# Optimization experiments

Measured on AMD Instinct MI355X. Metric: run time of the kernel, lower is better.

## Reference

```python
import jax, jax.numpy as jnp
import numpy as np

N = 100000          # nodes
E = 1600000         # edges (before self-loops)
IN = 128
H, C = 4, 32        # heads, out_channels per head
EPS = 1e-5          # BatchNorm eps
NEG_SLOPE = 0.2     # GATConv LeakyReLU slope


def setup_inputs() -> dict:
    key = jax.random.key(0)
    ks = jax.random.split(key, 8)
    return {
        "x": jax.random.normal(ks[0], (N, IN), jnp.float32),
        "edge_index": jax.random.randint(ks[1], (2, E), 0, N, dtype=jnp.int64),
        "W": jax.random.normal(ks[2], (IN, H * C), jnp.float32) * (1.0 / np.sqrt(IN)),
        "att_src": jax.random.normal(ks[3], (H, C), jnp.float32) * 0.1,
        "att_dst": jax.random.normal(ks[4], (H, C), jnp.float32) * 0.1,
        "bias": jax.random.normal(ks[5], (H * C,), jnp.float32) * 0.01,
        "gamma": jnp.ones((H * C,), jnp.float32),
        "beta": jnp.zeros((H * C,), jnp.float32),
    }


def reference(x, edge_index, W, att_src, att_dst, bias, gamma, beta):
    # --- GATConv (concat heads, add self-loops, eval-mode dropout) ---
    loop = jnp.arange(N, dtype=edge_index.dtype)
    src = jnp.concatenate([edge_index[0], loop])  # [E+N] message sources
    dst = jnp.concatenate([edge_index[1], loop])  # [E+N] message targets

    h = (x @ W).reshape(N, H, C)                       # [N,H,C]
    a_s = jnp.einsum('nhc,hc->nh', h, att_src)          # [N,H]
    a_d = jnp.einsum('nhc,hc->nh', h, att_dst)          # [N,H]

    e = a_s[src] + a_d[dst]                             # [E+N,H]
    e = jnp.where(e > 0, e, NEG_SLOPE * e)              # LeakyReLU

    # segment softmax over incoming edges of each dst node
    m = jax.ops.segment_max(e, dst, num_segments=N)     # [N,H]
    ex = jnp.exp(e - m[dst])
    den = jax.ops.segment_sum(ex, dst, num_segments=N)  # [N,H]
    alpha = ex / den[dst]                               # [E+N,H]

    out = jax.ops.segment_sum(h[src] * alpha[:, :, None], dst, num_segments=N)
    out = out.reshape(N, H * C) + bias                  # [N,128]

    # --- ELU activation ---
    out = jax.nn.elu(out)

    # --- BatchNorm1d (training-mode batch statistics, biased variance) ---
    mean = out.mean(axis=0)
    var = out.var(axis=0)
    return (out - mean) * jax.lax.rsqrt(var + EPS) * gamma + beta
```

## Files before the change

kernel.cpp:

```cpp
#include <hip/hip_runtime.h>

#define NEG 0.2f
#define MAXD 128
#define GEMM_BLOCKS 1024
#define COUNT_BLOCKS 2048

__device__ __forceinline__ float lrelu(float v) { return v > 0.f ? v : NEG * v; }

__device__ __forceinline__ unsigned f2bf(float f) {
  unsigned u = __float_as_uint(f);
  u = (u + 0x7FFFu + ((u >> 16) & 1u)) >> 16;
  return u;
}
__device__ __forceinline__ float bf_lo(unsigned u) { return __uint_as_float(u << 16); }
__device__ __forceinline__ float bf_hi(unsigned u) { return __uint_as_float(u & 0xFFFF0000u); }

typedef __attribute__((ext_vector_type(8))) short bf16x8;
typedef __attribute__((ext_vector_type(4))) float f32x4;

__global__ __launch_bounds__(256) void k_prep(const float* __restrict__ W,
                                              const float* __restrict__ att_src,
                                              const float* __restrict__ att_dst,
                                              unsigned short* __restrict__ Bext) {
  for (int id = blockIdx.x * 256 + threadIdx.x; id < 9 * 4 * 64 * 8; id += gridDim.x * 256) {
    int j = id & 7, lane = (id >> 3) & 63, kb = (id >> 9) & 3, ct = id >> 11;
    int k = kb * 32 + (lane >> 4) * 8 + j;
    int c = ct * 16 + (lane & 15);
    float v;
    if (c < 128) {
      v = W[k * 128 + c];
    } else {
      int slot = c - 128;
      int hd = slot & 3;
      const float* att = (slot < 4) ? att_src : att_dst;
      float s = 0.f;
      for (int jj = 0; jj < 32; ++jj) s = fmaf(W[k * 128 + hd * 32 + jj], att[hd * 32 + jj], s);
      v = s;
    }
    Bext[id] = (unsigned short)f2bf(v);
  }
}

__global__ __launch_bounds__(256) void k_gemm_count(
    const float* __restrict__ x, const unsigned short* __restrict__ Bext,
    unsigned* __restrict__ hb, float* __restrict__ a_s, float* __restrict__ a_d,
    int N, int ntiles,
    const int* __restrict__ ei, int* __restrict__ cnt8, int* __restrict__ rank,
    int E, int esh)
{
  const int tid = threadIdx.x;
  const int chunk = blockIdx.x >> 3;
  if (chunk % 3 == 0) {
    const int vb = (chunk / 3) * 8 + (blockIdx.x & 7);
    const bf16x8* Bfrag = reinterpret_cast<const bf16x8*>(Bext);
    const int w = tid >> 6, lane = tid & 63;
    const int r16 = lane & 15, g = lane >> 4;
    for (int tile = vb; tile < ntiles; tile += GEMM_BLOCKS) {
      int n0 = tile * 64 + w * 16;
      int rowc = min(n0 + r16, N - 1);
      const float* xp = x + (size_t)rowc * 128 + g * 8;
      bf16x8 afr[4];
#pragma unroll
      for (int kb = 0; kb < 4; ++kb) {
        float4 lo = *reinterpret_cast<const float4*>(xp + kb * 32);
        float4 hi = *reinterpret_cast<const float4*>(xp + kb * 32 + 4);
        bf16x8 t;
        t[0] = (short)f2bf(lo.x); t[1] = (short)f2bf(lo.y);
        t[2] = (short)f2bf(lo.z); t[3] = (short)f2bf(lo.w);
        t[4] = (short)f2bf(hi.x); t[5] = (short)f2bf(hi.y);
        t[6] = (short)f2bf(hi.z); t[7] = (short)f2bf(hi.w);
        afr[kb] = t;
      }
#pragma unroll
      for (int ct = 0; ct < 9; ++ct) {
        f32x4 acc = {0.f, 0.f, 0.f, 0.f};
#pragma unroll
        for (int kb = 0; kb < 4; ++kb) {
          bf16x8 bfr = Bfrag[(ct * 4 + kb) * 64 + lane];
          acc = __builtin_amdgcn_mfma_f32_16x16x32_bf16(afr[kb], bfr, acc, 0, 0, 0);
        }
        if (ct < 8) {
#pragma unroll
          for (int r = 0; r < 4; ++r) {
            int orow = n0 + g * 4 + r;
            unsigned b = f2bf(acc[r]);
            unsigned partner = __shfl_xor(b, 1);
            if (((lane & 1) == 0) && orow < N)
              hb[(size_t)orow * 64 + ct * 8 + (r16 >> 1)] = b | (partner << 16);
          }
        } else {
#pragma unroll
          for (int r = 0; r < 4; ++r) {
            int orow = n0 + g * 4 + r;
            if (r16 < 8 && orow < N) {
              if (r16 < 4) a_s[orow * 4 + r16] = acc[r];
              else         a_d[orow * 4 + (r16 - 4)] = acc[r];
            }
          }
        }
      }
    }
  } else {
    const int r = blockIdx.x & 7;
    const int cidx = chunk - 1 - (chunk / 3);
    const int qper = 1 << (esh - 2);
    const int ebase = r << esh;
    int* cpriv = cnt8 + (size_t)r * N;
    for (int ql = cidx * 256 + tid; ql < qper; ql += 256 * 256) {
      int e0 = ebase + (ql << 2);
      if (e0 >= E) break;
      if (e0 + 3 < E) {
        int4 d = *reinterpret_cast<const int4*>(ei + E + e0);
        int4 rk;
        rk.x = atomicAdd(&cpriv[d.x], 1);
        rk.y = atomicAdd(&cpriv[d.y], 1);
        rk.z = atomicAdd(&cpriv[d.z], 1);
        rk.w = atomicAdd(&cpriv[d.w], 1);
        *reinterpret_cast<int4*>(rank + e0) = rk;
      } else {
        for (int e = e0; e < E; ++e) {
          int d = ei[E + e];
          rank[e] = atomicAdd(&cpriv[d], 1);
        }
      }
    }
  }
}

__global__ __launch_bounds__(256) void k_scan1(int* __restrict__ cnt8, int* __restrict__ cnt,
                                               int* __restrict__ incl, int* __restrict__ bsum, int N) {
  __shared__ int sm[256];
  int i = blockIdx.x * 256 + threadIdx.x;
  int tot = 0;
  if (i < N) {
    int run = 0;
#pragma unroll
    for (int r = 0; r < 8; ++r) {
      int t = cnt8[(size_t)r * N + i];
      cnt8[(size_t)r * N + i] = run;
      run += t;
    }
    cnt[i] = run;
    tot = run;
  }
  sm[threadIdx.x] = tot;
  __syncthreads();
  for (int off = 1; off < 256; off <<= 1) {
    int t = (threadIdx.x >= off) ? sm[threadIdx.x - off] : 0;
    __syncthreads();
    sm[threadIdx.x] += t;
    __syncthreads();
  }
  if (i < N) incl[i] = sm[threadIdx.x];
  if (threadIdx.x == 255) bsum[blockIdx.x] = sm[255];
}

__global__ __launch_bounds__(512) void k_scan2(int* __restrict__ bsum, int nb) {
  __shared__ int sm[512];
  int v = (threadIdx.x < nb) ? bsum[threadIdx.x] : 0;
  sm[threadIdx.x] = v;
  __syncthreads();
  for (int off = 1; off < 512; off <<= 1) {
    int t = (threadIdx.x >= off) ? sm[threadIdx.x - off] : 0;
    __syncthreads();
    sm[threadIdx.x] += t;
    __syncthreads();
  }
  if (threadIdx.x < nb) bsum[threadIdx.x] = sm[threadIdx.x];
}

__global__ __launch_bounds__(256) void k_scan3(const int* __restrict__ cnt, const int* __restrict__ incl,
                                               const int* __restrict__ bsum, int* __restrict__ offs,
                                               int N, int E) {
  int i = blockIdx.x * 256 + threadIdx.x;
  if (i < N) {
    int base = (blockIdx.x > 0) ? bsum[blockIdx.x - 1] : 0;
    offs[i] = base + incl[i] - cnt[i];
  }
  if (i == 0) offs[N] = E;
}

__global__ __launch_bounds__(256) void k_scatter_rank(const int* __restrict__ ei,
                                                      const int* __restrict__ offs,
                                                      const int* __restrict__ cnt8,
                                                      const int* __restrict__ rank,
                                                      int* __restrict__ ssrc, int E, int rsize,
                                                      int esh, int N) {
  const int r = blockIdx.x & 7;
  const int lo = r * rsize, hi = lo + rsize;
  const int gtid = (blockIdx.x >> 3) * 256 + threadIdx.x;
  const int gstride = (gridDim.x >> 3) * 256;
  const int nquad = E >> 2;
  const int4* dst4 = reinterpret_cast<const int4*>(ei + E);
  for (int q = gtid; q < nquad; q += gstride) {
    int4 d = dst4[q];
    int e0 = q << 2;
    if (d.x >= lo && d.x < hi) ssrc[offs[d.x] + cnt8[(size_t)(e0 >> esh) * N + d.x] + rank[e0]]         = ei[e0];
    if (d.y >= lo && d.y < hi) ssrc[offs[d.y] + cnt8[(size_t)((e0+1) >> esh) * N + d.y] + rank[e0 + 1]] = ei[e0 + 1];
    if (d.z >= lo && d.z < hi) ssrc[offs[d.z] + cnt8[(size_t)((e0+2) >> esh) * N + d.z] + rank[e0 + 2]] = ei[e0 + 2];
    if (d.w >= lo && d.w < hi) ssrc[offs[d.w] + cnt8[(size_t)((e0+3) >> esh) * N + d.w] + rank[e0 + 3]] = ei[e0 + 3];
  }
  for (int e = (nquad << 2) + gtid; e < E; e += gstride) {
    int d = ei[E + e];
    if (d >= lo && d < hi) ssrc[offs[d] + cnt8[(size_t)(e >> esh) * N + d] + rank[e]] = ei[e];
  }
}

__global__ __launch_bounds__(256) void k_agg(
    const unsigned* __restrict__ hb, const float* __restrict__ a_s, const float* __restrict__ a_d,
    const int* __restrict__ offs, const int* __restrict__ ssrc,
    const float* __restrict__ bias, unsigned* __restrict__ preb,
    float* __restrict__ bnpart, int N)
{
  __shared__ float al[4][MAXD][4];
  __shared__ int   ls[4][MAXD];
  __shared__ float sv[4][128];
  const int wv = threadIdx.x >> 6;
  const int lane = threadIdx.x & 63;
  const int n = blockIdx.x * 4 + wv;

  if (n < N) {
    const int hsel = lane >> 4;
    const int start = offs[n], end = offs[n + 1];
    const int deg = end - start;
    const int jm = deg < MAXD ? deg : MAXD;
    float4 adv = *reinterpret_cast<const float4*>(&a_d[n * 4]);
    float4 asv = *reinterpret_cast<const float4*>(&a_s[n * 4]);
    float e0 = __expf(lrelu(asv.x + adv.x));
    float e1 = __expf(lrelu(asv.y + adv.y));
    float e2 = __expf(lrelu(asv.z + adv.z));
    float e3 = __expf(lrelu(asv.w + adv.w));
    float p0 = 0.f, p1 = 0.f, p2 = 0.f, p3 = 0.f;
    for (int j = lane; j < deg; j += 64) {
      int s = ssrc[start + j];
      float4 av = *reinterpret_cast<const float4*>(&a_s[s * 4]);
      float x0 = __expf(lrelu(av.x + adv.x));
      float x1 = __expf(lrelu(av.y + adv.y));
      float x2 = __expf(lrelu(av.z + adv.z));
      float x3 = __expf(lrelu(av.w + adv.w));
      p0 += x0; p1 += x1; p2 += x2; p3 += x3;
      if (j < MAXD) {
        float4 t = make_float4(x0, x1, x2, x3);
        *reinterpret_cast<float4*>(&al[wv][j][0]) = t;
        ls[wv][j] = s;
      }
    }
#pragma unroll
    for (int off = 32; off >= 1; off >>= 1) {
      p0 += __shfl_xor(p0, off);
      p1 += __shfl_xor(p1, off);
      p2 += __shfl_xor(p2, off);
      p3 += __shfl_xor(p3, off);
    }
    float rden0 = 1.f / (p0 + e0), rden1 = 1.f / (p1 + e1);
    float rden2 = 1.f / (p2 + e2), rden3 = 1.f / (p3 + e3);
    for (int j = lane; j < jm; j += 64) {
      float4 t = *reinterpret_cast<float4*>(&al[wv][j][0]);
      t.x *= rden0; t.y *= rden1; t.z *= rden2; t.w *= rden3;
      *reinterpret_cast<float4*>(&al[wv][j][0]) = t;
    }
    float ad_c = (hsel < 2) ? (hsel == 0 ? adv.x : adv.y) : (hsel == 2 ? adv.z : adv.w);
    float rden = (hsel < 2) ? (hsel == 0 ? rden0 : rden1) : (hsel == 2 ? rden2 : rden3);
    float esf = (hsel < 2) ? (hsel == 0 ? e0 : e1) : (hsel == 2 ? e2 : e3);
    unsigned us = hb[(size_t)n * 64 + lane];
    float wself = esf * rden;
    float acc0 = wself * bf_lo(us);
    float acc1 = wself * bf_hi(us);
    int j = 0;
    for (; j + 8 <= jm; j += 8) {
      int4 sA = *reinterpret_cast<int4*>(&ls[wv][j]);
      int4 sB = *reinterpret_cast<int4*>(&ls[wv][j + 4]);
      unsigned u0 = hb[(size_t)sA.x * 64 + lane];
      unsigned u1 = hb[(size_t)sA.y * 64 + lane];
      unsigned u2 = hb[(size_t)sA.z * 64 + lane];
      unsigned u3 = hb[(size_t)sA.w * 64 + lane];
      unsigned u4 = hb[(size_t)sB.x * 64 + lane];
      unsigned u5 = hb[(size_t)sB.y * 64 + lane];
      unsigned u6 = hb[(size_t)sB.z * 64 + lane];
      unsigned u7 = hb[(size_t)sB.w * 64 + lane];
      float w0 = al[wv][j][hsel];
      float w1 = al[wv][j + 1][hsel];
      float w2 = al[wv][j + 2][hsel];
      float w3 = al[wv][j + 3][hsel];
      float w4 = al[wv][j + 4][hsel];
      float w5 = al[wv][j + 5][hsel];
      float w6 = al[wv][j + 6][hsel];
      float w7 = al[wv][j + 7][hsel];
      acc0 = fmaf(w0, bf_lo(u0), acc0);
      acc1 = fmaf(w0, bf_hi(u0), acc1);
      acc0 = fmaf(w1, bf_lo(u1), acc0);
      acc1 = fmaf(w1, bf_hi(u1), acc1);
      acc0 = fmaf(w2, bf_lo(u2), acc0);
      acc1 = fmaf(w2, bf_hi(u2), acc1);
      acc0 = fmaf(w3, bf_lo(u3), acc0);
      acc1 = fmaf(w3, bf_hi(u3), acc1);
      acc0 = fmaf(w4, bf_lo(u4), acc0);
      acc1 = fmaf(w4, bf_hi(u4), acc1);
      acc0 = fmaf(w5, bf_lo(u5), acc0);
      acc1 = fmaf(w5, bf_hi(u5), acc1);
      acc0 = fmaf(w6, bf_lo(u6), acc0);
      acc1 = fmaf(w6, bf_hi(u6), acc1);
      acc0 = fmaf(w7, bf_lo(u7), acc0);
      acc1 = fmaf(w7, bf_hi(u7), acc1);
    }
    for (; j + 4 <= jm; j += 4) {
      int4 s4 = *reinterpret_cast<int4*>(&ls[wv][j]);
      unsigned u0 = hb[(size_t)s4.x * 64 + lane];
      unsigned u1 = hb[(size_t)s4.y * 64 + lane];
      unsigned u2 = hb[(size_t)s4.z * 64 + lane];
      unsigned u3 = hb[(size_t)s4.w * 64 + lane];
      float w0 = al[wv][j][hsel];
      float w1 = al[wv][j + 1][hsel];
      float w2 = al[wv][j + 2][hsel];
      float w3 = al[wv][j + 3][hsel];
      acc0 = fmaf(w0, bf_lo(u0), acc0);
      acc1 = fmaf(w0, bf_hi(u0), acc1);
      acc0 = fmaf(w1, bf_lo(u1), acc0);
      acc1 = fmaf(w1, bf_hi(u1), acc1);
      acc0 = fmaf(w2, bf_lo(u2), acc0);
      acc1 = fmaf(w2, bf_hi(u2), acc1);
      acc0 = fmaf(w3, bf_lo(u3), acc0);
      acc1 = fmaf(w3, bf_hi(u3), acc1);
    }
    for (; j < jm; ++j) {
      int s = ls[wv][j];
      float w = al[wv][j][hsel];
      unsigned u = hb[(size_t)s * 64 + lane];
      acc0 = fmaf(w, bf_lo(u), acc0);
      acc1 = fmaf(w, bf_hi(u), acc1);
    }
    for (int jj = MAXD; jj < deg; ++jj) {
      int s = ssrc[start + jj];
      float q = a_s[s * 4 + hsel];
      unsigned u = hb[(size_t)s * 64 + lane];
      float w = __expf(lrelu(q + ad_c)) * rden;
      acc0 = fmaf(w, bf_lo(u), acc0);
      acc1 = fmaf(w, bf_hi(u), acc1);
    }
    float2 bv = *reinterpret_cast<const float2*>(&bias[2 * lane]);
    float o0 = acc0 + bv.x;
    float o1 = acc1 + bv.y;
    o0 = o0 > 0.f ? o0 : expm1f(o0);
    o1 = o1 > 0.f ? o1 : expm1f(o1);
    preb[(size_t)n * 64 + lane] = f2bf(o0) | (f2bf(o1) << 16);
    sv[wv][2 * lane] = o0;
    sv[wv][2 * lane + 1] = o1;
  } else {
    sv[wv][2 * lane] = 0.f;
    sv[wv][2 * lane + 1] = 0.f;
  }
  __syncthreads();
  int t = threadIdx.x;
  if (t < 128) {
    float s = 0.f, q = 0.f;
#pragma unroll
    for (int w2 = 0; w2 < 4; ++w2) {
      float v = sv[w2][t];
      s += v;
      q = fmaf(v, v, q);
    }
    float* slot = bnpart + (size_t)(blockIdx.x & 63) * 256;
    atomicAdd(&slot[t], s);
    atomicAdd(&slot[128 + t], q);
  }
}

__global__ void k_bnfinal(const float* __restrict__ bnpart,
                          const float* __restrict__ gamma, const float* __restrict__ beta,
                          float* __restrict__ sc, float* __restrict__ sh, int N) {
  int c = threadIdx.x;
  float s = 0.f, q = 0.f;
  for (int p = 0; p < 64; ++p) {
    s += bnpart[p * 256 + c];
    q += bnpart[p * 256 + 128 + c];
  }
  float invn = 1.f / (float)N;
  float mean = s * invn;
  float var = q * invn - mean * mean;
  float scl = gamma[c] * rsqrtf(var + 1e-5f);
  sc[c] = scl;
  sh[c] = beta[c] - mean * scl;
}

__global__ __launch_bounds__(256) void k_bnapply(const unsigned* __restrict__ preb,
                                                 float* __restrict__ out,
                                                 const float* __restrict__ sc,
                                                 const float* __restrict__ sh, int npair2) {
  int i = blockIdx.x * blockDim.x + threadIdx.x;
  if (i >= npair2) return;
  uint2 u = reinterpret_cast<const uint2*>(preb)[i];
  int p0 = i * 2;
  int c0 = (p0 & 63) * 2;
  float4 scv = *reinterpret_cast<const float4*>(&sc[c0]);
  float4 shv = *reinterpret_cast<const float4*>(&sh[c0]);
  float4 v;
  v.x = fmaf(bf_lo(u.x), scv.x, shv.x);
  v.y = fmaf(bf_hi(u.x), scv.y, shv.y);
  v.z = fmaf(bf_lo(u.y), scv.z, shv.z);
  v.w = fmaf(bf_hi(u.y), scv.w, shv.w);
  reinterpret_cast<float4*>(out)[i] = v;
}

extern "C" void kernel_launch(void* const* d_in, const int* in_sizes, int n_in,
                              void* d_out, int out_size, void* d_ws, size_t ws_size,
                              hipStream_t stream) {
  const float* x = (const float*)d_in[0];
  const int* ei = (const int*)d_in[1];
  const float* W = (const float*)d_in[2];
  const float* att_src = (const float*)d_in[3];
  const float* att_dst = (const float*)d_in[4];
  const float* bias = (const float*)d_in[5];
  const float* gamma = (const float*)d_in[6];
  const float* beta = (const float*)d_in[7];
  float* out = (float*)d_out;

  const int N = in_sizes[0] / 128;
  const int E = in_sizes[1] / 2;

  char* ws = (char*)d_ws;
  size_t off = 0;
  auto alloc = [&](size_t bytes) {
    void* p = ws + off;
    off = (off + bytes + 255) & ~(size_t)255;
    return p;
  };
  unsigned* hb = (unsigned*)alloc((size_t)N * 64 * 4);
  float* a_s = (float*)alloc((size_t)N * 4 * 4);
  float* a_d = (float*)alloc((size_t)N * 4 * 4);
  int* cnt = (int*)alloc((size_t)N * 4);
  int* incl = (int*)alloc((size_t)N * 4);
  int* offs = (int*)alloc((size_t)(N + 1) * 4);
  int* bsum = (int*)alloc(512 * 4);
  int* rank = (int*)alloc((size_t)E * 4);
  int* ssrc = (int*)alloc((size_t)E * 4);
  unsigned* preb = (unsigned*)alloc((size_t)N * 64 * 4);
  float* bnpart = (float*)alloc(64 * 256 * 4);
  float* sc = (float*)alloc(128 * 4);
  float* sh = (float*)alloc(128 * 4);
  unsigned short* Bext = (unsigned short*)alloc(9 * 4 * 64 * 8 * 2);
  (void)n_in; (void)out_size; (void)ws_size;

  int* cnt8 = (int*)preb;

  int esh = 10;
  while (((E + (1 << esh) - 1) >> esh) > 8) ++esh;

  hipMemsetAsync(cnt8, 0, (size_t)N * 8 * 4, stream);
  hipMemsetAsync(bnpart, 0, 64 * 256 * 4, stream);

  k_prep<<<9, 256, 0, stream>>>(W, att_src, att_dst, Bext);

  int ntiles = (N + 63) / 64;
  k_gemm_count<<<GEMM_BLOCKS + COUNT_BLOCKS, 256, 0, stream>>>(
      x, Bext, hb, a_s, a_d, N, ntiles, ei, cnt8, rank, E, esh);

  int nb = (N + 255) / 256;
  k_scan1<<<nb, 256, 0, stream>>>(cnt8, cnt, incl, bsum, N);
  k_scan2<<<1, 512, 0, stream>>>(bsum, nb);
  k_scan3<<<nb, 256, 0, stream>>>(cnt, incl, bsum, offs, N, E);

  int rsize = (N + 7) / 8;
  k_scatter_rank<<<2048, 256, 0, stream>>>(ei, offs, cnt8, rank, ssrc, E, rsize, esh, N);

  k_agg<<<(N + 3) / 4, 256, 0, stream>>>(hb, a_s, a_d, offs, ssrc, bias, preb, bnpart, N);

  k_bnfinal<<<1, 128, 0, stream>>>(bnpart, gamma, beta, sc, sh, N);

  int npair2 = N * 32;
  k_bnapply<<<(npair2 + 255) / 256, 256, 0, stream>>>(preb, out, sc, sh, npair2);
}
```

Baseline: 234.0 us.

## Fuse memsets into prep, merge scan passes, fold offsets into per-slice counts

Replaces the two memset calls with zeroing loops inside the prep kernel, which now runs on 64 blocks. The second and third scan passes are merged into one kernel, where each block reduces the preceding block sums itself. That kernel also adds the node offset into each of the eight per-slice count arrays, so the scatter reads one index instead of two and loads ranks as int4. Together these cut launch count and global traffic in the CSR build, at the cost of each scan block doing a redundant reduction over up to about 390 block sums. The aggregation kernel also switches to 32-bit shift indexing for its gathers.

```diff
diff --git a/kernel.cpp b/kernel.cpp
--- a/kernel.cpp
+++ b/kernel.cpp
@@ -21,8 +21,12 @@
 __global__ __launch_bounds__(256) void k_prep(const float* __restrict__ W,
                                               const float* __restrict__ att_src,
                                               const float* __restrict__ att_dst,
-                                              unsigned short* __restrict__ Bext) {
-  for (int id = blockIdx.x * 256 + threadIdx.x; id < 9 * 4 * 64 * 8; id += gridDim.x * 256) {
+                                              unsigned short* __restrict__ Bext,
+                                              int* __restrict__ cnt8, float* __restrict__ bnpart,
+                                              int N) {
+  const int gtid = blockIdx.x * 256 + threadIdx.x;
+  const int gstride = gridDim.x * 256;
+  for (int id = gtid; id < 9 * 4 * 64 * 8; id += gstride) {
     int j = id & 7, lane = (id >> 3) & 63, kb = (id >> 9) & 3, ct = id >> 11;
     int k = kb * 32 + (lane >> 4) * 8 + j;
     int c = ct * 16 + (lane & 15);
@@ -39,6 +43,8 @@
     }
     Bext[id] = (unsigned short)f2bf(v);
   }
+  for (int i = gtid; i < N * 8; i += gstride) cnt8[i] = 0;
+  for (int i = gtid; i < 64 * 256; i += gstride) bnpart[i] = 0.f;
 }
 
 __global__ __launch_bounds__(256) void k_gemm_count(
@@ -86,7 +92,7 @@
             unsigned b = f2bf(acc[r]);
             unsigned partner = __shfl_xor(b, 1);
             if (((lane & 1) == 0) && orow < N)
-              hb[(size_t)orow * 64 + ct * 8 + (r16 >> 1)] = b | (partner << 16);
+              hb[((size_t)orow << 6) + ct * 8 + (r16 >> 1)] = b | (partner << 16);
           }
         } else {
 #pragma unroll
@@ -127,8 +133,8 @@
   }
 }
 
-__global__ __launch_bounds__(256) void k_scan1(int* __restrict__ cnt8, int* __restrict__ cnt,
-                                               int* __restrict__ incl, int* __restrict__ bsum, int N) {
+__global__ __launch_bounds__(256) void k_scan1(int* __restrict__ cnt8, int* __restrict__ excl,
+                                               int* __restrict__ bsum, int N) {
   __shared__ int sm[256];
   int i = blockIdx.x * 256 + threadIdx.x;
   int tot = 0;
@@ -140,7 +146,6 @@
       cnt8[(size_t)r * N + i] = run;
       run += t;
     }
-    cnt[i] = run;
     tot = run;
   }
   sm[threadIdx.x] = tot;
@@ -151,37 +156,36 @@
     sm[threadIdx.x] += t;
     __syncthreads();
   }
-  if (i < N) incl[i] = sm[threadIdx.x];
+  if (i < N) excl[i] = sm[threadIdx.x] - tot;
   if (threadIdx.x == 255) bsum[blockIdx.x] = sm[255];
 }
 
-__global__ __launch_bounds__(512) void k_scan2(int* __restrict__ bsum, int nb) {
-  __shared__ int sm[512];
-  int v = (threadIdx.x < nb) ? bsum[threadIdx.x] : 0;
-  sm[threadIdx.x] = v;
+__global__ __launch_bounds__(256) void k_scan23(const int* __restrict__ excl,
+                                                const int* __restrict__ bsum,
+                                                int* __restrict__ offs, int* __restrict__ cnt8,
+                                                int N, int E) {
+  __shared__ int red[256];
+  const int b = blockIdx.x;
+  int partial = 0;
+  for (int j = threadIdx.x; j < b; j += 256) partial += bsum[j];
+  red[threadIdx.x] = partial;
   __syncthreads();
-  for (int off = 1; off < 512; off <<= 1) {
-    int t = (threadIdx.x >= off) ? sm[threadIdx.x - off] : 0;
+  for (int off = 128; off >= 1; off >>= 1) {
+    if (threadIdx.x < off) red[threadIdx.x] += red[threadIdx.x + off];
     __syncthreads();
-    sm[threadIdx.x] += t;
-    __syncthreads();
-  }
-  if (threadIdx.x < nb) bsum[threadIdx.x] = sm[threadIdx.x];
-}
-
-__global__ __launch_bounds__(256) void k_scan3(const int* __restrict__ cnt, const int* __restrict__ incl,
-                                               const int* __restrict__ bsum, int* __restrict__ offs,
-                                               int N, int E) {
-  int i = blockIdx.x * 256 + threadIdx.x;
+  }
+  const int base = red[0];
+  int i = b * 256 + threadIdx.x;
   if (i < N) {
-    int base = (blockIdx.x > 0) ? bsum[blockIdx.x - 1] : 0;
-    offs[i] = base + incl[i] - cnt[i];
-  }
-  if (i == 0) offs[N] = E;
+    int o = base + excl[i];
+    offs[i] = o;
+#pragma unroll
+    for (int r = 0; r < 8; ++r) cnt8[(size_t)r * N + i] += o;
+  }
+  if (b == 0 && threadIdx.x == 0) offs[N] = E;
 }
 
 __global__ __launch_bounds__(256) void k_scatter_rank(const int* __restrict__ ei,
-                                                      const int* __restrict__ offs,
                                                       const int* __restrict__ cnt8,
                                                       const int* __restrict__ rank,
                                                       int* __restrict__ ssrc, int E, int rsize,
@@ -192,17 +196,20 @@
   const int gstride = (gridDim.x >> 3) * 256;
   const int nquad = E >> 2;
   const int4* dst4 = reinterpret_cast<const int4*>(ei + E);
+  const int4* rank4 = reinterpret_cast<const int4*>(rank);
   for (int q = gtid; q < nquad; q += gstride) {
     int4 d = dst4[q];
     int e0 = q << 2;
-    if (d.x >= lo && d.x < hi) ssrc[offs[d.x] + cnt8[(size_t)(e0 >> esh) * N + d.x] + rank[e0]]         = ei[e0];
-    if (d.y >= lo && d.y < hi) ssrc[offs[d.y] + cnt8[(size_t)((e0+1) >> esh) * N + d.y] + rank[e0 + 1]] = ei[e0 + 1];
-    if (d.z >= lo && d.z < hi) ssrc[offs[d.z] + cnt8[(size_t)((e0+2) >> esh) * N + d.z] + rank[e0 + 2]] = ei[e0 + 2];
-    if (d.w >= lo && d.w < hi) ssrc[offs[d.w] + cnt8[(size_t)((e0+3) >> esh) * N + d.w] + rank[e0 + 3]] = ei[e0 + 3];
+    const int* sub = cnt8 + (size_t)(e0 >> esh) * N;
+    int4 rk = rank4[q];
+    if (d.x >= lo && d.x < hi) ssrc[sub[d.x] + rk.x] = ei[e0];
+    if (d.y >= lo && d.y < hi) ssrc[sub[d.y] + rk.y] = ei[e0 + 1];
+    if (d.z >= lo && d.z < hi) ssrc[sub[d.z] + rk.z] = ei[e0 + 2];
+    if (d.w >= lo && d.w < hi) ssrc[sub[d.w] + rk.w] = ei[e0 + 3];
   }
   for (int e = (nquad << 2) + gtid; e < E; e += gstride) {
     int d = ei[E + e];
-    if (d >= lo && d < hi) ssrc[offs[d] + cnt8[(size_t)(e >> esh) * N + d] + rank[e]] = ei[e];
+    if (d >= lo && d < hi) ssrc[cnt8[(size_t)(e >> esh) * N + d] + rank[e]] = ei[e];
   }
 }
 
@@ -262,7 +269,7 @@
     float ad_c = (hsel < 2) ? (hsel == 0 ? adv.x : adv.y) : (hsel == 2 ? adv.z : adv.w);
     float rden = (hsel < 2) ? (hsel == 0 ? rden0 : rden1) : (hsel == 2 ? rden2 : rden3);
     float esf = (hsel < 2) ? (hsel == 0 ? e0 : e1) : (hsel == 2 ? e2 : e3);
-    unsigned us = hb[(size_t)n * 64 + lane];
+    unsigned us = hb[((unsigned)n << 6) + lane];
     float wself = esf * rden;
     float acc0 = wself * bf_lo(us);
     float acc1 = wself * bf_hi(us);
@@ -270,14 +277,14 @@
     for (; j + 8 <= jm; j += 8) {
       int4 sA = *reinterpret_cast<int4*>(&ls[wv][j]);
       int4 sB = *reinterpret_cast<int4*>(&ls[wv][j + 4]);
-      unsigned u0 = hb[(size_t)sA.x * 64 + lane];
-      unsigned u1 = hb[(size_t)sA.y * 64 + lane];
-      unsigned u2 = hb[(size_t)sA.z * 64 + lane];
-      unsigned u3 = hb[(size_t)sA.w * 64 + lane];
-      unsigned u4 = hb[(size_t)sB.x * 64 + lane];
-      unsigned u5 = hb[(size_t)sB.y * 64 + lane];
-      unsigned u6 = hb[(size_t)sB.z * 64 + lane];
-      unsigned u7 = hb[(size_t)sB.w * 64 + lane];
+      unsigned u0 = hb[((unsigned)sA.x << 6) + lane];
+      unsigned u1 = hb[((unsigned)sA.y << 6) + lane];
+      unsigned u2 = hb[((unsigned)sA.z << 6) + lane];
+      unsigned u3 = hb[((unsigned)sA.w << 6) + lane];
+      unsigned u4 = hb[((unsigned)sB.x << 6) + lane];
+      unsigned u5 = hb[((unsigned)sB.y << 6) + lane];
+      unsigned u6 = hb[((unsigned)sB.z << 6) + lane];
+      unsigned u7 = hb[((unsigned)sB.w << 6) + lane];
       float w0 = al[wv][j][hsel];
       float w1 = al[wv][j + 1][hsel];
       float w2 = al[wv][j + 2][hsel];
@@ -305,10 +312,10 @@
     }
     for (; j + 4 <= jm; j += 4) {
       int4 s4 = *reinterpret_cast<int4*>(&ls[wv][j]);
-      unsigned u0 = hb[(size_t)s4.x * 64 + lane];
-      unsigned u1 = hb[(size_t)s4.y * 64 + lane];
-      unsigned u2 = hb[(size_t)s4.z * 64 + lane];
-      unsigned u3 = hb[(size_t)s4.w * 64 + lane];
+      unsigned u0 = hb[((unsigned)s4.x << 6) + lane];
+      unsigned u1 = hb[((unsigned)s4.y << 6) + lane];
+      unsigned u2 = hb[((unsigned)s4.z << 6) + lane];
+      unsigned u3 = hb[((unsigned)s4.w << 6) + lane];
       float w0 = al[wv][j][hsel];
       float w1 = al[wv][j + 1][hsel];
       float w2 = al[wv][j + 2][hsel];
@@ -325,14 +332,14 @@
     for (; j < jm; ++j) {
       int s = ls[wv][j];
       float w = al[wv][j][hsel];
-      unsigned u = hb[(size_t)s * 64 + lane];
+      unsigned u = hb[((unsigned)s << 6) + lane];
       acc0 = fmaf(w, bf_lo(u), acc0);
       acc1 = fmaf(w, bf_hi(u), acc1);
     }
     for (int jj = MAXD; jj < deg; ++jj) {
       int s = ssrc[start + jj];
       float q = a_s[s * 4 + hsel];
-      unsigned u = hb[(size_t)s * 64 + lane];
+      unsigned u = hb[((unsigned)s << 6) + lane];
       float w = __expf(lrelu(q + ad_c)) * rden;
       acc0 = fmaf(w, bf_lo(u), acc0);
       acc1 = fmaf(w, bf_hi(u), acc1);
@@ -342,7 +349,7 @@
     float o1 = acc1 + bv.y;
     o0 = o0 > 0.f ? o0 : expm1f(o0);
     o1 = o1 > 0.f ? o1 : expm1f(o1);
-    preb[(size_t)n * 64 + lane] = f2bf(o0) | (f2bf(o1) << 16);
+    preb[((size_t)n << 6) + lane] = f2bf(o0) | (f2bf(o1) << 16);
     sv[wv][2 * lane] = o0;
     sv[wv][2 * lane + 1] = o1;
   } else {
@@ -427,8 +434,7 @@
   unsigned* hb = (unsigned*)alloc((size_t)N * 64 * 4);
   float* a_s = (float*)alloc((size_t)N * 4 * 4);
   float* a_d = (float*)alloc((size_t)N * 4 * 4);
-  int* cnt = (int*)alloc((size_t)N * 4);
-  int* incl = (int*)alloc((size_t)N * 4);
+  int* excl = (int*)alloc((size_t)N * 4);
   int* offs = (int*)alloc((size_t)(N + 1) * 4);
   int* bsum = (int*)alloc(512 * 4);
   int* rank = (int*)alloc((size_t)E * 4);
@@ -445,22 +451,18 @@
   int esh = 10;
   while (((E + (1 << esh) - 1) >> esh) > 8) ++esh;
 
-  hipMemsetAsync(cnt8, 0, (size_t)N * 8 * 4, stream);
-  hipMemsetAsync(bnpart, 0, 64 * 256 * 4, stream);
-
-  k_prep<<<9, 256, 0, stream>>>(W, att_src, att_dst, Bext);
+  k_prep<<<64, 256, 0, stream>>>(W, att_src, att_dst, Bext, cnt8, bnpart, N);
 
   int ntiles = (N + 63) / 64;
   k_gemm_count<<<GEMM_BLOCKS + COUNT_BLOCKS, 256, 0, stream>>>(
       x, Bext, hb, a_s, a_d, N, ntiles, ei, cnt8, rank, E, esh);
 
   int nb = (N + 255) / 256;
-  k_scan1<<<nb, 256, 0, stream>>>(cnt8, cnt, incl, bsum, N);
-  k_scan2<<<1, 512, 0, stream>>>(bsum, nb);
-  k_scan3<<<nb, 256, 0, stream>>>(cnt, incl, bsum, offs, N, E);
+  k_scan1<<<nb, 256, 0, stream>>>(cnt8, excl, bsum, N);
+  k_scan23<<<nb, 256, 0, stream>>>(excl, bsum, offs, cnt8, N, E);
 
   int rsize = (N + 7) / 8;
-  k_scatter_rank<<<2048, 256, 0, stream>>>(ei, offs, cnt8, rank, ssrc, E, rsize, esh, N);
+  k_scatter_rank<<<2048, 256, 0, stream>>>(ei, cnt8, rank, ssrc, E, rsize, esh, N);
 
   k_agg<<<(N + 3) / 4, 256, 0, stream>>>(hb, a_s, a_d, offs, ssrc, bias, preb, bnpart, N);
 
```

Measured after the change: 219.7 us. 6.1% less time.
